# Kernel optimization log

Hardware: AMD Instinct MI355X
Metric: run time of the kernel (lower is better)

The kernel has to match this reference:

```python
import jax, jax.numpy as jnp
import numpy as np

C = 1.0          # curvature
MIN_NORM = 1e-15
EPS = 1e-7       # atanh clamp for fp32

def _sqnorm(x):
    return jnp.sum(x * x, axis=-1, keepdims=True)

def _norm(x):
    return jnp.sqrt(jnp.maximum(_sqnorm(x), MIN_NORM))

def _atanh(u):
    return jnp.arctanh(jnp.clip(u, -1.0 + EPS, 1.0 - EPS))

def mobius_add(x, y, c):
    x2 = _sqnorm(x); y2 = _sqnorm(y)
    xy = jnp.sum(x * y, axis=-1, keepdims=True)
    num = (1.0 + 2.0 * c * xy + c * y2) * x + (1.0 - c * x2) * y
    den = 1.0 + 2.0 * c * xy + c * c * x2 * y2
    return num / jnp.maximum(den, MIN_NORM)

def logmap0(p, c):
    sc = jnp.sqrt(c)
    pn = _norm(p)
    return p / pn / sc * _atanh(sc * pn)

def logmap(p1, p2, c):
    # tangent vector at p1 pointing to p2 (Poincare ball)
    sub = mobius_add(-p1, p2, c)
    sn = _norm(sub)
    lam = 2.0 / jnp.maximum(1.0 - c * _sqnorm(p1), MIN_NORM)
    sc = jnp.sqrt(c)
    return 2.0 / sc / lam * _atanh(sc * sn) * sub / sn

def expmap(p, u, c):
    un = _norm(u)
    lam = 2.0 / jnp.maximum(1.0 - c * _sqnorm(p), MIN_NORM)
    sc = jnp.sqrt(c)
    second = jnp.tanh(sc * lam * un / 2.0) * u / (sc * un)
    return mobius_add(p, second, c)


def setup_inputs() -> dict:
    key = jax.random.key(0)
    k1, k2, k3 = jax.random.split(key, 3)
    B, N, D = 1, 1024, 128
    # points inside the unit Poincare ball (||x|| ~ 0.23)
    x = jax.random.normal(k1, (B, N, D), jnp.float32) * 0.02
    # sparse-ish dense adjacency mask (0/1 floats)
    adj = (jax.random.uniform(k2, (B, N, N)) < 0.05).astype(jnp.float32)
    # DenseAtt: nn.Linear(2*D, 1) weight (flattened) + bias
    att_w = jax.random.normal(k3, (2 * D,), jnp.float32) * 0.1
    att_b = jnp.zeros((), jnp.float32)
    return {"x": x, "adj": adj, "att_w": att_w, "att_b": att_b}


def reference(x, adj, att_w, att_b):
    B, N, D = x.shape
    x_t = logmap0(x, C)                                   # [B,N,D]
    # DenseAtt: sigmoid(Linear(cat(x_i, x_j))) decomposed as left_i + right_j + b
    left = x_t @ att_w[:D]                                # [B,N]
    right = x_t @ att_w[D:]                               # [B,N]
    att = jax.nn.sigmoid(left[:, :, None] + right[:, None, :] + att_b) * adj  # [B,N,N]
    # pairwise logmap: tangent at x_i of every x_j  -> [B,N,N,D]
    x_local = logmap(x[:, :, None, :], x[:, None, :, :], C)
    support_t = jnp.einsum('bij,bijd->bid', att, x_local)  # [B,N,D]
    return expmap(x, support_t, C)
```

## Files before the change

### kernel.cpp

```cpp
#include <hip/hip_runtime.h>
#include <math.h>


typedef short short4v __attribute__((ext_vector_type(4)));
typedef short short8v __attribute__((ext_vector_type(8)));
typedef float float4v __attribute__((ext_vector_type(4)));

static __device__ __forceinline__ short f2bf(float f) {
    unsigned u = __float_as_uint(f);
    u += 0x7fff + ((u >> 16) & 1);
    return (short)(u >> 16);
}
static __device__ __forceinline__ float rcpf(float x) { return __builtin_amdgcn_rcpf(x); }

__global__ __launch_bounds__(256) void hyp_stats(
    const float* __restrict__ x, const float* __restrict__ w,
    float* __restrict__ st_x2, float* __restrict__ st_L, float* __restrict__ st_R)
{
    int row  = blockIdx.x * 4 + (threadIdx.x >> 6);
    int lane = threadIdx.x & 63;
    const float* xr = x + row * 128;
    float a0 = xr[lane], a1 = xr[lane + 64];
    float x2 = a0 * a0 + a1 * a1;
    float dl = a0 * w[lane]       + a1 * w[lane + 64];
    float dr = a0 * w[lane + 128] + a1 * w[lane + 192];
    for (int m = 1; m < 64; m <<= 1) {
        x2 += __shfl_xor(x2, m);
        dl += __shfl_xor(dl, m);
        dr += __shfl_xor(dr, m);
    }
    if (lane == 0) {
        float pn = sqrtf(fmaxf(x2, 1e-15f));
        float uu = fminf(pn, 1.f - 1e-7f);
        float at = 0.5f * __logf((1.f + uu) * rcpf(1.f - uu));
        float f  = at * rcpf(pn);
        st_x2[row] = x2;
        st_L[row]  = f * dl;
        st_R[row]  = f * dr;
    }
}

__global__ __launch_bounds__(256) void hyp_main(
    const float* __restrict__ x, const float* __restrict__ adj,
    const float* __restrict__ battp,
    const float* __restrict__ st_x2, const float* __restrict__ st_L,
    const float* __restrict__ st_R,
    float* __restrict__ Y, float* __restrict__ Sg)
{
    __shared__ unsigned short sXI[16 * 132];
    __shared__ unsigned short sXJ[128 * 132];
    __shared__ unsigned short sW [16 * 132];
    __shared__ float sAdj[16 * 129];
    __shared__ float sX2J[128], sRJ[128];
    __shared__ float sX2I[16], sLI[16], sBI[16];
    __shared__ float sS[16];

    const int t    = threadIdx.x;
    const int lane = t & 63;
    const int wave = t >> 6;
    const int n    = lane & 15;
    const int q    = lane >> 4;
    const int i0   = blockIdx.x * 16;
    const int j0   = blockIdx.y * 256;
    const float batt = battp[0];

    if (t < 16) {
        float v = st_x2[i0 + t];
        sX2I[t] = v; sBI[t] = 1.f - v; sLI[t] = st_L[i0 + t];
        sS[t] = 0.f;
    }
    for (int idx = t; idx < 16 * 32; idx += 256) {
        int r = idx >> 5, c = idx & 31;
        float4v v = ((const float4v*)x)[(i0 + r) * 32 + c];
        short4v h = { f2bf(v[0]), f2bf(v[1]), f2bf(v[2]), f2bf(v[3]) };
        *(short4v*)&sXI[r * 132 + c * 4] = h;
    }
    __syncthreads();

    float x2i4[4], bi4[4], li4[4];
    for (int r = 0; r < 4; ++r) {
        int i = q * 4 + r;
        x2i4[r] = sX2I[i]; bi4[r] = sBI[i]; li4[r] = sLI[i];
    }
    short8v afrag[4];
    for (int kk = 0; kk < 4; ++kk) {
        const unsigned short* p = &sXI[n * 132 + kk * 32 + q * 8];
        short4v lo = *(const short4v*)p;
        short4v hi = *(const short4v*)(p + 4);
        afrag[kk] = (short8v){ lo[0], lo[1], lo[2], lo[3], hi[0], hi[1], hi[2], hi[3] };
    }

    float4v accB[2];
    accB[0] = (float4v){0.f, 0.f, 0.f, 0.f};
    accB[1] = (float4v){0.f, 0.f, 0.f, 0.f};
    float Sacc[4] = {0.f, 0.f, 0.f, 0.f};

    for (int half = 0; half < 2; ++half) {
        const int jh = j0 + half * 128;
        __syncthreads();
        for (int idx = t; idx < 128 * 32; idx += 256) {
            int r = idx >> 5, c = idx & 31;
            float4v v = ((const float4v*)x)[(jh + r) * 32 + c];
            short4v h = { f2bf(v[0]), f2bf(v[1]), f2bf(v[2]), f2bf(v[3]) };
            *(short4v*)&sXJ[r * 132 + c * 4] = h;
        }
        for (int idx = t; idx < 16 * 32; idx += 256) {
            int r = idx >> 5, c = idx & 31;
            float4v v = ((const float4v*)adj)[(i0 + r) * 256 + (jh >> 2) + c];
            float* d = &sAdj[r * 129 + c * 4];
            d[0] = v[0]; d[1] = v[1]; d[2] = v[2]; d[3] = v[3];
        }
        if (t < 128) { sX2J[t] = st_x2[jh + t]; sRJ[t] = st_R[jh + t]; }
        __syncthreads();

        for (int jsl = 0; jsl < 2; ++jsl) {
            int js = wave * 2 + jsl;
            int jrow = js * 16 + n;
            float4v acc = (float4v){0.f, 0.f, 0.f, 0.f};
            for (int kk = 0; kk < 4; ++kk) {
                const unsigned short* p = &sXJ[jrow * 132 + kk * 32 + q * 8];
                short4v lo = *(const short4v*)p;
                short4v hi = *(const short4v*)(p + 4);
                short8v b = (short8v){ lo[0], lo[1], lo[2], lo[3], hi[0], hi[1], hi[2], hi[3] };
                acc = __builtin_amdgcn_mfma_f32_16x16x32_bf16(afrag[kk], b, acc, 0, 0, 0);
            }
            float x2j = sX2J[js * 16 + n];
            float rj  = sRJ[js * 16 + n];
            for (int r = 0; r < 4; ++r) {
                float G    = acc[r];
                int   i    = q * 4 + r;
                float adjv = sAdj[i * 129 + js * 16 + n];
                float alpha = 1.f - 2.f * G + x2j;
                float den   = fmaxf(fmaf(x2i4[r], x2j, 1.f - 2.f * G), 1e-15f);
                float rdn   = rcpf(den);
                float bb    = bi4[r];
                float nn2   = alpha * alpha * x2i4[r] + bb * bb * x2j - 2.f * alpha * bb * G;
                float sub2  = nn2 * rdn * rdn;
                float sn    = sqrtf(fmaxf(sub2, 1e-15f));
                float uu    = fminf(sn, 1.f - 1e-7f);
                float at    = 0.5f * __logf((1.f + uu) * rcpf(1.f - uu));
                float tt    = at * rcpf(sn);
                float z     = li4[r] + rj + batt;
                float sig   = rcpf(1.f + __expf(-z));
                float g     = sig * adjv * tt * rdn;
                Sacc[r]     = fmaf(g, alpha, Sacc[r]);
                sW[i * 132 + js * 16 + n] = (unsigned short)f2bf(g);
            }
        }
        __syncthreads();

        for (int nsl = 0; nsl < 2; ++nsl) {
            int ns = wave * 2 + nsl;
            for (int kk = 0; kk < 4; ++kk) {
                const unsigned short* pa = &sW[n * 132 + kk * 32 + q * 8];
                short4v lo = *(const short4v*)pa;
                short4v hi = *(const short4v*)(pa + 4);
                short8v a = (short8v){ lo[0], lo[1], lo[2], lo[3], hi[0], hi[1], hi[2], hi[3] };
                short8v b;
                int kbase = kk * 32 + q * 8;
#pragma unroll
                for (int e = 0; e < 8; ++e)
                    b[e] = (short)sXJ[(kbase + e) * 132 + ns * 16 + n];
                accB[nsl] = __builtin_amdgcn_mfma_f32_16x16x32_bf16(a, b, accB[nsl], 0, 0, 0);
            }
        }
    }

    for (int r = 0; r < 4; ++r) {
        float v = Sacc[r];
        v += __shfl_xor(v, 1); v += __shfl_xor(v, 2);
        v += __shfl_xor(v, 4); v += __shfl_xor(v, 8);
        if (n == 0) atomicAdd(&sS[q * 4 + r], v);
    }
    for (int nsl = 0; nsl < 2; ++nsl) {
        int ns = wave * 2 + nsl;
        for (int r = 0; r < 4; ++r)
            atomicAdd(&Y[(i0 + q * 4 + r) * 128 + ns * 16 + n], accB[nsl][r]);
    }
    __syncthreads();
    if (t < 16) atomicAdd(&Sg[i0 + t], sS[t]);
}

__global__ __launch_bounds__(256) void hyp_exp(
    const float* __restrict__ x, const float* __restrict__ Y,
    const float* __restrict__ Sg, const float* __restrict__ st_x2,
    float* __restrict__ out)
{
    int i    = blockIdx.x * 4 + (threadIdx.x >> 6);
    int lane = threadIdx.x & 63;
    float x0 = x[i * 128 + lane], x1 = x[i * 128 + 64 + lane];
    float y0 = Y[i * 128 + lane], y1 = Y[i * 128 + 64 + lane];
    float S  = Sg[i];
    float x2 = st_x2[i];
    float b  = fmaxf(1.f - x2, 1e-15f);
    float u0 = b * (b * y0 - S * x0);
    float u1 = b * (b * y1 - S * x1);
    float un2 = u0 * u0 + u1 * u1;
    float xu  = x0 * u0 + x1 * u1;
    for (int m = 1; m < 64; m <<= 1) {
        un2 += __shfl_xor(un2, m);
        xu  += __shfl_xor(xu, m);
    }
    float un  = sqrtf(fmaxf(un2, 1e-15f));
    float th  = tanhf(un * rcpf(b));
    float s2  = th * rcpf(un);
    float xy  = s2 * xu;
    float y2s = th * th;
    float coef = 1.f + 2.f * xy + y2s;
    float den  = fmaxf(1.f + 2.f * xy + x2 * y2s, 1e-15f);
    float rd   = rcpf(den);
    out[i * 128 + lane]      = (coef * x0 + b * (s2 * u0)) * rd;
    out[i * 128 + 64 + lane] = (coef * x1 + b * (s2 * u1)) * rd;
}

extern "C" void kernel_launch(void* const* d_in, const int* in_sizes, int n_in,
                              void* d_out, int out_size, void* d_ws, size_t ws_size,
                              hipStream_t stream) {
    const float* x    = (const float*)d_in[0];
    const float* adj  = (const float*)d_in[1];
    const float* w    = (const float*)d_in[2];
    const float* batt = (const float*)d_in[3];
    float* out = (float*)d_out;

    float* Y     = (float*)d_ws;
    float* Sg    = Y + 131072;
    float* st_x2 = Sg + 1024;
    float* st_L  = st_x2 + 1024;
    float* st_R  = st_L + 1024;

    hipMemsetAsync(d_ws, 0, (131072 + 1024) * sizeof(float), stream);
    hipLaunchKernelGGL(hyp_stats, dim3(256), dim3(256), 0, stream, x, w, st_x2, st_L, st_R);
    hipLaunchKernelGGL(hyp_main, dim3(64, 4), dim3(256), 0, stream,
                       x, adj, batt, st_x2, st_L, st_R, Y, Sg);
    hipLaunchKernelGGL(hyp_exp, dim3(256), dim3(256), 0, stream, x, Y, Sg, st_x2, out);
}
```

Measured before the change: 83.61 us.

## Replace atomics and memset with per-chunk partials, add transposed XJ tile

The main kernel now splits j into 8 chunks of 128, one per block, and drops the inner half loop. Each block writes its own partial Y and S slices, and the exp kernel sums them, which removes the global atomics and the workspace memset. The j tile is also stored transposed in shared memory so the second MFMA reads B fragments with vector loads instead of strided scalar loads. Adjacency and the per-row stats are read straight from global into registers, and tanh is replaced with an exp-based formula. The cost is more shared memory, more workspace, and an 8-way reduction in the final kernel.

Measured after the change: 73.29 us. 1.14x faster.

```diff
diff --git a/kernel.cpp b/kernel.cpp
--- a/kernel.cpp
+++ b/kernel.cpp
@@ -12,6 +12,11 @@
     return (short)(u >> 16);
 }
 static __device__ __forceinline__ float rcpf(float x) { return __builtin_amdgcn_rcpf(x); }
+static __device__ __forceinline__ short8v ld8(const unsigned short* p) {
+    short4v lo = *(const short4v*)p;
+    short4v hi = *(const short4v*)(p + 4);
+    return (short8v){lo[0],lo[1],lo[2],lo[3],hi[0],hi[1],hi[2],hi[3]};
+}
 
 __global__ __launch_bounds__(256) void hyp_stats(
     const float* __restrict__ x, const float* __restrict__ w,
@@ -40,19 +45,17 @@
     }
 }
 
-__global__ __launch_bounds__(256) void hyp_main(
+__global__ __launch_bounds__(256, 2) void hyp_main(
     const float* __restrict__ x, const float* __restrict__ adj,
     const float* __restrict__ battp,
     const float* __restrict__ st_x2, const float* __restrict__ st_L,
     const float* __restrict__ st_R,
-    float* __restrict__ Y, float* __restrict__ Sg)
+    float* __restrict__ Yp, float* __restrict__ Sp)
 {
-    __shared__ unsigned short sXI[16 * 132];
-    __shared__ unsigned short sXJ[128 * 132];
-    __shared__ unsigned short sW [16 * 132];
-    __shared__ float sAdj[16 * 129];
-    __shared__ float sX2J[128], sRJ[128];
-    __shared__ float sX2I[16], sLI[16], sBI[16];
+    __shared__ unsigned short sXI [16 * 132];
+    __shared__ unsigned short sXJ [128 * 132];
+    __shared__ unsigned short sXJt[128 * 132];
+    __shared__ unsigned short sW  [16 * 132];
     __shared__ float sS[16];
 
     const int t    = threadIdx.x;
@@ -61,136 +64,151 @@
     const int n    = lane & 15;
     const int q    = lane >> 4;
     const int i0   = blockIdx.x * 16;
-    const int j0   = blockIdx.y * 256;
+    const int c    = blockIdx.y;
+    const int j0   = c * 128;
     const float batt = battp[0];
 
-    if (t < 16) {
-        float v = st_x2[i0 + t];
-        sX2I[t] = v; sBI[t] = 1.f - v; sLI[t] = st_L[i0 + t];
-        sS[t] = 0.f;
-    }
+    float x2i4[4], bi4[4], li4[4];
+#pragma unroll
+    for (int r = 0; r < 4; ++r) {
+        int i = i0 + q * 4 + r;
+        x2i4[r] = st_x2[i];
+        li4[r]  = st_L[i];
+    }
+    float x2j2[2], rj2[2], adjv[2][4];
+#pragma unroll
+    for (int jsl = 0; jsl < 2; ++jsl) {
+        int j = j0 + (wave * 2 + jsl) * 16 + n;
+        x2j2[jsl] = st_x2[j];
+        rj2[jsl]  = st_R[j];
+#pragma unroll
+        for (int r = 0; r < 4; ++r)
+            adjv[jsl][r] = adj[(i0 + q * 4 + r) * 1024 + j];
+    }
+#pragma unroll
+    for (int r = 0; r < 4; ++r) bi4[r] = 1.f - x2i4[r];
+
+    if (t < 16) sS[t] = 0.f;
+
     for (int idx = t; idx < 16 * 32; idx += 256) {
-        int r = idx >> 5, c = idx & 31;
-        float4v v = ((const float4v*)x)[(i0 + r) * 32 + c];
+        int r = idx >> 5, cc = idx & 31;
+        float4v v = ((const float4v*)x)[(i0 + r) * 32 + cc];
         short4v h = { f2bf(v[0]), f2bf(v[1]), f2bf(v[2]), f2bf(v[3]) };
-        *(short4v*)&sXI[r * 132 + c * 4] = h;
+        *(short4v*)&sXI[r * 132 + cc * 4] = h;
+    }
+#pragma unroll
+    for (int it = 0; it < 4; ++it) {
+        int bid = t + it * 256;
+        int jr = ((bid >> 4) & 3) | (((bid >> 6) & 7) << 2);
+        int dc = (bid & 15) | (((bid >> 9) & 1) << 4);
+        float4v v[4];
+#pragma unroll
+        for (int e = 0; e < 4; ++e)
+            v[e] = ((const float4v*)x)[(j0 + jr * 4 + e) * 32 + dc];
+        short4v h[4];
+#pragma unroll
+        for (int e = 0; e < 4; ++e) {
+            h[e] = (short4v){ f2bf(v[e][0]), f2bf(v[e][1]), f2bf(v[e][2]), f2bf(v[e][3]) };
+            *(short4v*)&sXJ[(jr * 4 + e) * 132 + dc * 4] = h[e];
+        }
+#pragma unroll
+        for (int d = 0; d < 4; ++d) {
+            short4v ht = (short4v){ h[0][d], h[1][d], h[2][d], h[3][d] };
+            *(short4v*)&sXJt[(dc * 4 + d) * 132 + jr * 4] = ht;
+        }
     }
     __syncthreads();
 
-    float x2i4[4], bi4[4], li4[4];
-    for (int r = 0; r < 4; ++r) {
-        int i = q * 4 + r;
-        x2i4[r] = sX2I[i]; bi4[r] = sBI[i]; li4[r] = sLI[i];
-    }
     short8v afrag[4];
-    for (int kk = 0; kk < 4; ++kk) {
-        const unsigned short* p = &sXI[n * 132 + kk * 32 + q * 8];
-        short4v lo = *(const short4v*)p;
-        short4v hi = *(const short4v*)(p + 4);
-        afrag[kk] = (short8v){ lo[0], lo[1], lo[2], lo[3], hi[0], hi[1], hi[2], hi[3] };
-    }
+#pragma unroll
+    for (int kk = 0; kk < 4; ++kk)
+        afrag[kk] = ld8(&sXI[n * 132 + kk * 32 + q * 8]);
+
+    float Sacc[4] = {0.f, 0.f, 0.f, 0.f};
+
+#pragma unroll
+    for (int jsl = 0; jsl < 2; ++jsl) {
+        int js = wave * 2 + jsl;
+        int jrow = js * 16 + n;
+        float4v acc = (float4v){0.f, 0.f, 0.f, 0.f};
+#pragma unroll
+        for (int kk = 0; kk < 4; ++kk) {
+            short8v b = ld8(&sXJ[jrow * 132 + kk * 32 + q * 8]);
+            acc = __builtin_amdgcn_mfma_f32_16x16x32_bf16(afrag[kk], b, acc, 0, 0, 0);
+        }
+        float x2j = x2j2[jsl];
+        float rj  = rj2[jsl];
+#pragma unroll
+        for (int r = 0; r < 4; ++r) {
+            float G     = acc[r];
+            int   i     = q * 4 + r;
+            float alpha = 1.f - 2.f * G + x2j;
+            float den   = fmaxf(fmaf(x2i4[r], x2j, 1.f - 2.f * G), 1e-15f);
+            float rdn   = rcpf(den);
+            float bb    = bi4[r];
+            float nn2   = alpha * alpha * x2i4[r] + bb * bb * x2j - 2.f * alpha * bb * G;
+            float sub2  = nn2 * rdn * rdn;
+            float sn    = sqrtf(fmaxf(sub2, 1e-15f));
+            float uu    = fminf(sn, 1.f - 1e-7f);
+            float at    = 0.5f * __logf((1.f + uu) * rcpf(1.f - uu));
+            float tt    = at * rcpf(sn);
+            float z     = li4[r] + rj + batt;
+            float sig   = rcpf(1.f + __expf(-z));
+            float g     = sig * adjv[jsl][r] * tt * rdn;
+            Sacc[r]     = fmaf(g, alpha, Sacc[r]);
+            sW[i * 132 + js * 16 + n] = (unsigned short)f2bf(g);
+        }
+    }
+    __syncthreads();
 
     float4v accB[2];
     accB[0] = (float4v){0.f, 0.f, 0.f, 0.f};
     accB[1] = (float4v){0.f, 0.f, 0.f, 0.f};
-    float Sacc[4] = {0.f, 0.f, 0.f, 0.f};
-
-    for (int half = 0; half < 2; ++half) {
-        const int jh = j0 + half * 128;
-        __syncthreads();
-        for (int idx = t; idx < 128 * 32; idx += 256) {
-            int r = idx >> 5, c = idx & 31;
-            float4v v = ((const float4v*)x)[(jh + r) * 32 + c];
-            short4v h = { f2bf(v[0]), f2bf(v[1]), f2bf(v[2]), f2bf(v[3]) };
-            *(short4v*)&sXJ[r * 132 + c * 4] = h;
-        }
-        for (int idx = t; idx < 16 * 32; idx += 256) {
-            int r = idx >> 5, c = idx & 31;
-            float4v v = ((const float4v*)adj)[(i0 + r) * 256 + (jh >> 2) + c];
-            float* d = &sAdj[r * 129 + c * 4];
-            d[0] = v[0]; d[1] = v[1]; d[2] = v[2]; d[3] = v[3];
-        }
-        if (t < 128) { sX2J[t] = st_x2[jh + t]; sRJ[t] = st_R[jh + t]; }
-        __syncthreads();
-
-        for (int jsl = 0; jsl < 2; ++jsl) {
-            int js = wave * 2 + jsl;
-            int jrow = js * 16 + n;
-            float4v acc = (float4v){0.f, 0.f, 0.f, 0.f};
-            for (int kk = 0; kk < 4; ++kk) {
-                const unsigned short* p = &sXJ[jrow * 132 + kk * 32 + q * 8];
-                short4v lo = *(const short4v*)p;
-                short4v hi = *(const short4v*)(p + 4);
-                short8v b = (short8v){ lo[0], lo[1], lo[2], lo[3], hi[0], hi[1], hi[2], hi[3] };
-                acc = __builtin_amdgcn_mfma_f32_16x16x32_bf16(afrag[kk], b, acc, 0, 0, 0);
-            }
-            float x2j = sX2J[js * 16 + n];
-            float rj  = sRJ[js * 16 + n];
-            for (int r = 0; r < 4; ++r) {
-                float G    = acc[r];
-                int   i    = q * 4 + r;
-                float adjv = sAdj[i * 129 + js * 16 + n];
-                float alpha = 1.f - 2.f * G + x2j;
-                float den   = fmaxf(fmaf(x2i4[r], x2j, 1.f - 2.f * G), 1e-15f);
-                float rdn   = rcpf(den);
-                float bb    = bi4[r];
-                float nn2   = alpha * alpha * x2i4[r] + bb * bb * x2j - 2.f * alpha * bb * G;
-                float sub2  = nn2 * rdn * rdn;
-                float sn    = sqrtf(fmaxf(sub2, 1e-15f));
-                float uu    = fminf(sn, 1.f - 1e-7f);
-                float at    = 0.5f * __logf((1.f + uu) * rcpf(1.f - uu));
-                float tt    = at * rcpf(sn);
-                float z     = li4[r] + rj + batt;
-                float sig   = rcpf(1.f + __expf(-z));
-                float g     = sig * adjv * tt * rdn;
-                Sacc[r]     = fmaf(g, alpha, Sacc[r]);
-                sW[i * 132 + js * 16 + n] = (unsigned short)f2bf(g);
-            }
-        }
-        __syncthreads();
-
-        for (int nsl = 0; nsl < 2; ++nsl) {
-            int ns = wave * 2 + nsl;
-            for (int kk = 0; kk < 4; ++kk) {
-                const unsigned short* pa = &sW[n * 132 + kk * 32 + q * 8];
-                short4v lo = *(const short4v*)pa;
-                short4v hi = *(const short4v*)(pa + 4);
-                short8v a = (short8v){ lo[0], lo[1], lo[2], lo[3], hi[0], hi[1], hi[2], hi[3] };
-                short8v b;
-                int kbase = kk * 32 + q * 8;
-#pragma unroll
-                for (int e = 0; e < 8; ++e)
-                    b[e] = (short)sXJ[(kbase + e) * 132 + ns * 16 + n];
-                accB[nsl] = __builtin_amdgcn_mfma_f32_16x16x32_bf16(a, b, accB[nsl], 0, 0, 0);
-            }
-        }
-    }
-
+#pragma unroll
+    for (int nsl = 0; nsl < 2; ++nsl) {
+        int ns = wave * 2 + nsl;
+#pragma unroll
+        for (int kk = 0; kk < 4; ++kk) {
+            short8v a = ld8(&sW  [n * 132 + kk * 32 + q * 8]);
+            short8v b = ld8(&sXJt[(ns * 16 + n) * 132 + kk * 32 + q * 8]);
+            accB[nsl] = __builtin_amdgcn_mfma_f32_16x16x32_bf16(a, b, accB[nsl], 0, 0, 0);
+        }
+    }
+
+#pragma unroll
     for (int r = 0; r < 4; ++r) {
         float v = Sacc[r];
         v += __shfl_xor(v, 1); v += __shfl_xor(v, 2);
         v += __shfl_xor(v, 4); v += __shfl_xor(v, 8);
         if (n == 0) atomicAdd(&sS[q * 4 + r], v);
     }
+    float* Yc = Yp + c * 131072;
+#pragma unroll
     for (int nsl = 0; nsl < 2; ++nsl) {
         int ns = wave * 2 + nsl;
+#pragma unroll
         for (int r = 0; r < 4; ++r)
-            atomicAdd(&Y[(i0 + q * 4 + r) * 128 + ns * 16 + n], accB[nsl][r]);
+            Yc[(i0 + q * 4 + r) * 128 + ns * 16 + n] = accB[nsl][r];
     }
     __syncthreads();
-    if (t < 16) atomicAdd(&Sg[i0 + t], sS[t]);
+    if (t < 16) Sp[c * 1024 + i0 + t] = sS[t];
 }
 
 __global__ __launch_bounds__(256) void hyp_exp(
-    const float* __restrict__ x, const float* __restrict__ Y,
-    const float* __restrict__ Sg, const float* __restrict__ st_x2,
+    const float* __restrict__ x, const float* __restrict__ Yp,
+    const float* __restrict__ Sp, const float* __restrict__ st_x2,
     float* __restrict__ out)
 {
     int i    = blockIdx.x * 4 + (threadIdx.x >> 6);
     int lane = threadIdx.x & 63;
+    float y0 = 0.f, y1 = 0.f, S = 0.f;
+#pragma unroll
+    for (int cc = 0; cc < 8; ++cc) {
+        y0 += Yp[cc * 131072 + i * 128 + lane];
+        y1 += Yp[cc * 131072 + i * 128 + 64 + lane];
+        S  += Sp[cc * 1024 + i];
+    }
     float x0 = x[i * 128 + lane], x1 = x[i * 128 + 64 + lane];
-    float y0 = Y[i * 128 + lane], y1 = Y[i * 128 + 64 + lane];
-    float S  = Sg[i];
     float x2 = st_x2[i];
     float b  = fmaxf(1.f - x2, 1e-15f);
     float u0 = b * (b * y0 - S * x0);
@@ -202,7 +220,8 @@
         xu  += __shfl_xor(xu, m);
     }
     float un  = sqrtf(fmaxf(un2, 1e-15f));
-    float th  = tanhf(un * rcpf(b));
+    float e2  = __expf(2.f * un * rcpf(b));
+    float th  = 1.f - 2.f * rcpf(e2 + 1.f);
     float s2  = th * rcpf(un);
     float xy  = s2 * xu;
     float y2s = th * th;
@@ -222,15 +241,14 @@
     const float* batt = (const float*)d_in[3];
     float* out = (float*)d_out;
 
-    float* Y     = (float*)d_ws;
-    float* Sg    = Y + 131072;
-    float* st_x2 = Sg + 1024;
+    float* Yp    = (float*)d_ws;
+    float* Sp    = Yp + 8 * 131072;
+    float* st_x2 = Sp + 8 * 1024;
     float* st_L  = st_x2 + 1024;
     float* st_R  = st_L + 1024;
 
-    hipMemsetAsync(d_ws, 0, (131072 + 1024) * sizeof(float), stream);
     hipLaunchKernelGGL(hyp_stats, dim3(256), dim3(256), 0, stream, x, w, st_x2, st_L, st_R);
-    hipLaunchKernelGGL(hyp_main, dim3(64, 4), dim3(256), 0, stream,
-                       x, adj, batt, st_x2, st_L, st_R, Y, Sg);
-    hipLaunchKernelGGL(hyp_exp, dim3(256), dim3(256), 0, stream, x, Y, Sg, st_x2, out);
-}
+    hipLaunchKernelGGL(hyp_main, dim3(64, 8), dim3(256), 0, stream,
+                       x, adj, batt, st_x2, st_L, st_R, Yp, Sp);
+    hipLaunchKernelGGL(hyp_exp, dim3(256), dim3(256), 0, stream, x, Yp, Sp, st_x2, out);
+}
```
